# Optimization experiments

Hardware: AMD Instinct MI355X
Metric: run time of the kernel (lower is better)

## Reference

```python
import jax, jax.numpy as jnp
import numpy as np

WS = 7           # window_size
DIM_HEAD = 32    # qk head dim
NUM_HEAD = 8     # dim_in // dim_head = 256 // 32
DIM_EXP = 1024   # dim_in * exp_ratio
WIN_NUM = 16     # (28 // 7) ** 2
EPS = 1e-5


def _rel_pos_index():
    # same construction as torch buffer; returns [49*49] int index into (2*WS-1)^2 table
    coords = np.stack(np.meshgrid(np.arange(WS), np.arange(WS), indexing='ij'))  # [2,WS,WS]
    cf = coords.reshape(2, -1)                                                   # [2,49]
    rel = cf[:, :, None] - cf[:, None, :]                                        # [2,49,49]
    rel = rel.transpose(1, 2, 0)
    rel[:, :, 0] += WS - 1
    rel[:, :, 1] += WS - 1
    rel[:, :, 0] *= 2 * WS - 1
    return jnp.asarray(rel.sum(-1).reshape(-1), dtype=jnp.int32)                 # [2401]


def _ln_channel(x, w, b):
    # LayerNorm over channel dim (axis=1) of [b,c,h,w], per the 'ln_1d' norm
    mu = jnp.mean(x, axis=1, keepdims=True)
    var = jnp.var(x, axis=1, keepdims=True)
    xn = (x - mu) * jax.lax.rsqrt(var + EPS)
    return xn * w[None, :, None, None] + b[None, :, None, None]


def setup_inputs() -> dict:
    key = jax.random.key(0)
    ks = jax.random.split(key, 12)
    C = 256
    x = jax.random.normal(ks[0], (64, C, 28, 28), dtype=jnp.float32)
    return {
        'x': x,
        'pre_w': jnp.ones((C,), jnp.float32),
        'pre_b': jnp.zeros((C,), jnp.float32),
        'qk_w': jax.random.normal(ks[1], (2 * C, C), jnp.float32) * 0.02,
        'qk_b': jnp.zeros((2 * C,), jnp.float32),
        'v_w': jax.random.normal(ks[2], (DIM_EXP, C), jnp.float32) * 0.02,
        'v_b': jnp.zeros((DIM_EXP,), jnp.float32),
        'post_w': jnp.ones((DIM_EXP // 2,), jnp.float32),
        'post_b': jnp.zeros((DIM_EXP // 2,), jnp.float32),
        'proj_w': jax.random.normal(ks[3], (C, DIM_EXP), jnp.float32) * 0.02,
        'proj_b': jnp.zeros((C,), jnp.float32),
        'rpb_table': jax.random.normal(ks[4], (WIN_NUM, (2 * WS - 1) ** 2, NUM_HEAD), jnp.float32) * 0.02,
    }


def reference(x, pre_w, pre_b, qk_w, qk_b, v_w, v_b, post_w, post_b, proj_w, proj_b, rpb_table):
    B, C, H, W = x.shape
    n1, n2 = H // WS, W // WS
    shortcut = x
    # b c (h1 n1) (w1 n2) -> (b n1 n2) c h1 w1
    xw = x.reshape(B, C, WS, n1, WS, n2).transpose(0, 3, 5, 1, 2, 4).reshape(B * n1 * n2, C, WS, WS)
    b = B * n1 * n2
    xw = _ln_channel(xw, pre_w, pre_b)
    # 1x1 conv QK -> split into q,k per head: channels ordered (qk, heads, dim_head)
    qk = jnp.einsum('oc,bchw->bohw', qk_w, xw) + qk_b[None, :, None, None]
    qk = qk.reshape(b, 2, NUM_HEAD, DIM_HEAD, WS * WS).transpose(1, 0, 2, 4, 3)  # [2,b,h,49,dh]
    q, k = qk[0], qk[1]
    # 1x1 conv V -> attn half + idle half
    v = jnp.einsum('oc,bchw->bohw', v_w, xw) + v_b[None, :, None, None]
    v_attn, v_idle = jnp.split(v, 2, axis=1)                                     # each [b,512,7,7]
    dhv = (DIM_EXP // 2) // NUM_HEAD
    va = v_attn.reshape(b, NUM_HEAD, dhv, WS * WS).transpose(0, 1, 3, 2)         # [b,h,49,dhv]
    # relative position bias (gathered fresh each forward, one table per window)
    idx = _rel_pos_index()
    bias = rpb_table[:, idx, :]                                                  # [wn,2401,nh]
    bias = bias.reshape(WIN_NUM, WS * WS, WS * WS, NUM_HEAD).transpose(0, 3, 1, 2)
    bias = jnp.broadcast_to(bias[None], (B, WIN_NUM, NUM_HEAD, WS * WS, WS * WS)).reshape(b, NUM_HEAD, WS * WS, WS * WS)
    # SDPA (scale = 1/sqrt(q head dim), additive float mask)
    scale = DIM_HEAD ** -0.5
    logits = jnp.einsum('bhqd,bhkd->bhqk', q, k) * scale + bias
    attn = jax.nn.softmax(logits, axis=-1)
    out = jnp.einsum('bhqk,bhkd->bhqd', attn, va)                                # [b,h,49,dhv]
    out = out.transpose(0, 1, 3, 2).reshape(b, DIM_EXP // 2, WS, WS)
    out = _ln_channel(out, post_w, post_b)
    xc = jnp.concatenate([out, v_idle], axis=1)                                  # [b,dim_exp,7,7]
    # (b n1 n2) c h1 w1 -> b c (h1 n1) (w1 n2)
    xc = xc.reshape(B, n1, n2, DIM_EXP, WS, WS).transpose(0, 3, 4, 1, 5, 2).reshape(B, DIM_EXP, H, W)
    xc = jax.nn.gelu(xc, approximate=False)
    xc = jnp.einsum('oc,bchw->bohw', proj_w, xc) + proj_b[None, :, None, None]
    y = shortcut + xc
    return jnp.roll(y, shift=(2, 2), axis=(2, 3))
```

## Files before the change

kernel.cpp:

```cpp
#include <hip/hip_runtime.h>
#include <hip/hip_bf16.h>

typedef __bf16          bf16x8 __attribute__((ext_vector_type(8)));
typedef float           f32x4  __attribute__((ext_vector_type(4)));
typedef unsigned int    u32x2  __attribute__((ext_vector_type(2)));
typedef unsigned int    u32x4v __attribute__((ext_vector_type(4)));

#define QKW_OFF  0
#define VW_OFF   262144
#define PJW_OFF  786432
#define BIAS_OFF 1310720
#define XT_OFF   70516736

#define MFMA(a,b,c) __builtin_amdgcn_mfma_f32_16x16x32_bf16((a),(b),(c),0,0,0)
#define ZERO4 ((f32x4){0.f,0.f,0.f,0.f})
#define CBAR() asm volatile("" ::: "memory")

#define SXN_AT(row, byte)      ((((row)*512 + (byte))) ^ ((((row)&7))<<4))
#define RGB(j)                 (25088 + (j)*6400)
#define RG_AT(base, row, byte) (((base) + (row)*128 + (byte)) ^ (((row)&7)<<4))
#define SC_AT(row, byte)       ((25088 + (row)*512 + (byte)) ^ (((row)&7)<<4))

static __device__ __forceinline__ unsigned cvtpk(float lo, float hi){
  unsigned r;
  asm("v_cvt_pk_bf16_f32 %0, %1, %2" : "=v"(r) : "v"(lo), "v"(hi));
  return r;
}
static __device__ __forceinline__ unsigned short f2bu(float f) {
  unsigned u = __builtin_bit_cast(unsigned, f);
  return (unsigned short)((u + 0x7FFFu + ((u >> 16) & 1u)) >> 16);
}
static __device__ __forceinline__ float gelu_f(float v){
  return v / (1.f + __expf(-1.5957691216057308f*v*(1.f + 0.044715f*v*v)));
}

__global__ void emo_prep_wb(const float* __restrict__ qk_w, const float* __restrict__ v_w,
                            const float* __restrict__ proj_w, const float* __restrict__ rpb,
                            unsigned short* __restrict__ w16, float* __restrict__ bx) {
  const int blk = blockIdx.x;
  if (blk < 2560) {
    int i = blk * 256 + threadIdx.x;
    if (i >= 655360) return;
    float v;
    if (i < 131072)      v = qk_w[i];
    else if (i < 393216) v = v_w[i - 131072];
    else                 v = proj_w[i - 393216];
    unsigned u = __builtin_bit_cast(unsigned, v);
    w16[i] = (unsigned short)((u + 0x7FFFu + ((u >> 16) & 1u)) >> 16);
  } else {
    const int wh = blk - 2560;
    const int win = wh >> 3, h = wh & 7;
    for (int e = threadIdx.x; e < 4096; e += 256) {
      const int chunk = e >> 8, lane = (e >> 2) & 63, r = e & 3;
      const int mt = chunk >> 2, nt = chunk & 3;
      const int m = mt*16 + (lane >> 4)*4 + r;
      const int n = nt*16 + (lane & 15);
      float v;
      if (n >= 49)      v = -1e30f;
      else if (m >= 49) v = 0.f;
      else {
        const int dI = m/7 - n/7 + 6;
        const int dJ = m%7 - n%7 + 6;
        v = rpb[(win*169 + dI*13 + dJ)*8 + h];
      }
      bx[wh*4096 + e] = v;
    }
  }
}

__global__ __launch_bounds__(256)
void emo_prep_x(const float* __restrict__ x, const float* __restrict__ pre_w,
                const float* __restrict__ pre_b, unsigned short* __restrict__ xt) {
  __shared__ float lv[32*257];
  __shared__ float ps1[8][32];
  __shared__ float ps2[8][32];
  const int tid = threadIdx.x, lane = tid & 63, wv = tid >> 6;
  const int l32 = lane & 31, hp = lane >> 5;
  const int chunk = blockIdx.x, b = blockIdx.y;
  const int s = chunk*32 + l32;
  const bool ok = s < 784;
  const float* xb = x + (size_t)b*200704;
  float s1 = 0.f, s2 = 0.f;
  const int c0 = wv*64 + hp*32;
  for (int ci = 0; ci < 32; ++ci) {
    const int c = c0 + ci;
    const float v = ok ? xb[c*784 + s] : 0.f;
    lv[l32*257 + c] = v;
    s1 += v; s2 += v*v;
  }
  ps1[wv*2 + hp][l32] = s1;
  ps2[wv*2 + hp][l32] = s2;
  __syncthreads();
  const int px = tid & 31, j = tid >> 5;
  const int sp = chunk*32 + px;
  if (sp < 784) {
    float t1 = 0.f, t2 = 0.f;
    #pragma unroll
    for (int k = 0; k < 8; ++k) { t1 += ps1[k][px]; t2 += ps2[k][px]; }
    const float mu = t1*(1.f/256.f);
    const float rs = rsqrtf(t2*(1.f/256.f) - mu*mu + 1e-5f);
    const int h = sp/28, w = sp - h*28;
    const int win = (h & 3)*4 + (w & 3);
    const int wpx = (h >> 2)*7 + (w >> 2);
    unsigned short* row = xt + (((size_t)b*16 + win)*49 + wpx)*256 + j*32;
    #pragma unroll
    for (int g = 0; g < 4; ++g) {
      float gg[8];
      #pragma unroll
      for (int i2 = 0; i2 < 8; ++i2) {
        const int c = j*32 + g*8 + i2;
        gg[i2] = (lv[px*257 + c] - mu)*rs*pre_w[c] + pre_b[c];
      }
      u32x4v pk = { cvtpk(gg[0],gg[1]), cvtpk(gg[2],gg[3]), cvtpk(gg[4],gg[5]), cvtpk(gg[6],gg[7]) };
      *(u32x4v*)(row + g*8) = pk;
    }
  }
}

__global__ __launch_bounds__(512, 4)
void emo_main(const float* __restrict__ x,
              const float* __restrict__ qk_b,  const float* __restrict__ v_b,
              const float* __restrict__ post_w,const float* __restrict__ post_b,
              const float* __restrict__ proj_b,
              const char*  __restrict__ wsc,
              float* __restrict__ out)
{
  extern __shared__ char smem[];
  const int tid  = threadIdx.x;
  const int lane = tid & 63;
  const int l16  = lane & 15;
  const int lk   = lane >> 4;
  const int wv   = tid >> 6;
  const int bid  = blockIdx.x;
  const int Bi   = (bid & 7) * 8 + (bid >> 7);
  const int win  = (bid >> 3) & 15;
  const int n1   = win >> 2, n2 = win & 3;
  const size_t xbase = (size_t)Bi * (256*784);
  const int SCR  = RGB(wv);

  {
    const unsigned short* xw = (const unsigned short*)(wsc + XT_OFF)
                             + ((size_t)Bi*16 + win)*(49*256);
    for (int p = wv; p < 49; p += 8) {
      const u32x2 d = *(const u32x2*)(xw + p*256 + lane*4);
      *(u32x2*)(smem + SXN_AT(p, lane*8)) = d;
    }
  }
  __syncthreads();

  f32x4 aq[2][4], ak[2][4];
  #pragma unroll
  for (int mt = 0; mt < 2; ++mt)
    #pragma unroll
    for (int nt = 0; nt < 4; ++nt) { aq[mt][nt] = ZERO4; ak[mt][nt] = ZERO4; }
  #pragma unroll 2
  for (int kt = 0; kt < 8; ++kt) {
    bf16x8 bx[4];
    #pragma unroll
    for (int nt = 0; nt < 4; ++nt) {
      const int row = nt*16 + l16, rc = row < 49 ? row : 48;
      bx[nt] = *(const bf16x8*)(smem + SXN_AT(rc, kt*64 + lk*16));
    }
    #pragma unroll
    for (int mt = 0; mt < 2; ++mt) {
      const bf16x8 awq = *(const bf16x8*)(wsc + QKW_OFF + (size_t)(      wv*32 + mt*16 + l16)*512 + kt*64 + lk*16);
      const bf16x8 awk = *(const bf16x8*)(wsc + QKW_OFF + (size_t)(256 + wv*32 + mt*16 + l16)*512 + kt*64 + lk*16);
      #pragma unroll
      for (int nt = 0; nt < 4; ++nt) {
        aq[mt][nt] = MFMA(awq, bx[nt], aq[mt][nt]);
        ak[mt][nt] = MFMA(awk, bx[nt], ak[mt][nt]);
      }
    }
  }
  {
    const f32x4 bq0 = *(const f32x4*)(qk_b +       wv*32 +      lk*4);
    const f32x4 bq1 = *(const f32x4*)(qk_b +       wv*32 + 16 + lk*4);
    const f32x4 bk0 = *(const f32x4*)(qk_b + 256 + wv*32 +      lk*4);
    const f32x4 bk1 = *(const f32x4*)(qk_b + 256 + wv*32 + 16 + lk*4);
    #pragma unroll
    for (int nt = 0; nt < 4; ++nt) {
      aq[0][nt] += bq0; aq[1][nt] += bq1; ak[0][nt] += bk0; ak[1][nt] += bk1;
    }
  }

  #pragma unroll
  for (int nt = 0; nt < 4; ++nt) {
    const int px = nt*16 + l16;
    if (px < 49) {
      #pragma unroll
      for (int mt = 0; mt < 2; ++mt) {
        u32x2 pq  = { cvtpk(aq[mt][nt][0], aq[mt][nt][1]), cvtpk(aq[mt][nt][2], aq[mt][nt][3]) };
        u32x2 pk2 = { cvtpk(ak[mt][nt][0], ak[mt][nt][1]), cvtpk(ak[mt][nt][2], ak[mt][nt][3]) };
        *(u32x2*)(smem + RG_AT(SCR, px,      (mt*16 + lk*4)*2)) = pq;
        *(u32x2*)(smem + RG_AT(SCR, px, 64 + (mt*16 + lk*4)*2)) = pk2;
      }
    }
  }
  CBAR();

  bf16x8 qa[4], kb[4];
  #pragma unroll
  for (int t = 0; t < 4; ++t) {
    const int row = t*16 + l16, rc = row < 49 ? row : 48;
    qa[t] = *(const bf16x8*)(smem + RG_AT(SCR, rc,      lk*16));
    kb[t] = *(const bf16x8*)(smem + RG_AT(SCR, rc, 64 + lk*16));
  }

  f32x4 s[4][4];
  {
    const float scale = 0.17677669529663689f;
    const float* bxp = (const float*)(wsc + BIAS_OFF) + (size_t)(win*8 + wv)*4096 + lane*4;
    #pragma unroll
    for (int mt = 0; mt < 4; ++mt)
      #pragma unroll
      for (int nt = 0; nt < 4; ++nt) {
        f32x4 z = MFMA(qa[mt], kb[nt], ZERO4);
        s[mt][nt] = z*scale + *(const f32x4*)(bxp + (mt*4 + nt)*256);
      }
  }
  #pragma unroll
  for (int mt = 0; mt < 4; ++mt) {
    #pragma unroll
    for (int r = 0; r < 4; ++r) {
      float mx = fmaxf(fmaxf(s[mt][0][r], s[mt][1][r]), fmaxf(s[mt][2][r], s[mt][3][r]));
      mx = fmaxf(mx, __shfl_xor(mx, 1)); mx = fmaxf(mx, __shfl_xor(mx, 2));
      mx = fmaxf(mx, __shfl_xor(mx, 4)); mx = fmaxf(mx, __shfl_xor(mx, 8));
      const float e0 = __expf(s[mt][0][r]-mx), e1 = __expf(s[mt][1][r]-mx);
      const float e2 = __expf(s[mt][2][r]-mx), e3 = __expf(s[mt][3][r]-mx);
      float sm = e0+e1+e2+e3;
      sm += __shfl_xor(sm, 1); sm += __shfl_xor(sm, 2);
      sm += __shfl_xor(sm, 4); sm += __shfl_xor(sm, 8);
      const float inv = 1.f/sm;
      s[mt][0][r] = e0*inv; s[mt][1][r] = e1*inv;
      s[mt][2][r] = e2*inv; s[mt][3][r] = e3*inv;
    }
  }
  #pragma unroll
  for (int mt = 0; mt < 4; ++mt)
    #pragma unroll
    for (int r = 0; r < 4; ++r) {
      const int q = mt*16 + lk*4 + r;
      if (q < 49) {
        #pragma unroll
        for (int nt = 0; nt < 4; ++nt)
          *(unsigned short*)(smem + RG_AT(SCR, q, (nt*16 + l16)*2)) = f2bu(s[mt][nt][r]);
      }
    }
  CBAR();

  f32x4 av[4][4];
  #pragma unroll
  for (int mt = 0; mt < 4; ++mt)
    #pragma unroll
    for (int nt = 0; nt < 4; ++nt) av[mt][nt] = ZERO4;
  #pragma unroll 2
  for (int kt = 0; kt < 8; ++kt) {
    bf16x8 ax[4], bw[4];
    #pragma unroll
    for (int t = 0; t < 4; ++t) {
      const int row = t*16 + l16, rc = row < 49 ? row : 48;
      ax[t] = *(const bf16x8*)(smem + SXN_AT(rc, kt*64 + lk*16));
      bw[t] = *(const bf16x8*)(wsc + VW_OFF + (size_t)(wv*64 + t*16 + l16)*512 + kt*64 + lk*16);
    }
    #pragma unroll
    for (int mt = 0; mt < 4; ++mt)
      #pragma unroll
      for (int nt = 0; nt < 4; ++nt) av[mt][nt] = MFMA(ax[mt], bw[nt], av[mt][nt]);
  }
  {
    #pragma unroll
    for (int nt = 0; nt < 4; ++nt) {
      const float vb = v_b[wv*64 + nt*16 + l16];
      #pragma unroll
      for (int mt = 0; mt < 4; ++mt)
        #pragma unroll
        for (int r = 0; r < 4; ++r) av[mt][nt][r] += vb;
    }
  }

  bf16x8 fpb[4][2];
  #pragma unroll
  for (int t = 0; t < 4; ++t) {
    const int row = t*16 + l16, rc = row < 49 ? row : 48;
    #pragma unroll
    for (int kt = 0; kt < 2; ++kt)
      fpb[t][kt] = *(const bf16x8*)(smem + RG_AT(SCR, rc, (kt*32 + lk*8)*2));
  }
  CBAR();

  f32x4 o[4][4];
  #pragma unroll
  for (int h2 = 0; h2 < 2; ++h2) {
    #pragma unroll
    for (int tc = 0; tc < 2; ++tc) {
      const int nt = h2*2 + tc;
      const int chrow = tc*16 + l16;
      #pragma unroll
      for (int mt = 0; mt < 4; ++mt) {
        u32x2 pv = { cvtpk(av[mt][nt][0], av[mt][nt][1]), cvtpk(av[mt][nt][2], av[mt][nt][3]) };
        *(u32x2*)(smem + RG_AT(SCR, chrow, (mt*16 + lk*4)*2)) = pv;
      }
    }
    CBAR();
    #pragma unroll
    for (int tc = 0; tc < 2; ++tc) {
      const int mtc = h2*2 + tc;
      const bf16x8 a0 = *(const bf16x8*)(smem + RG_AT(SCR, tc*16 + l16, (     lk*8)*2));
      const bf16x8 a1 = *(const bf16x8*)(smem + RG_AT(SCR, tc*16 + l16, (32 + lk*8)*2));
      #pragma unroll
      for (int nt = 0; nt < 4; ++nt) {
        f32x4 z = MFMA(a0, fpb[nt][0], ZERO4);
        o[mtc][nt] = MFMA(a1, fpb[nt][1], z);
      }
    }
    CBAR();
  }

  #pragma unroll
  for (int mtc = 0; mtc < 4; ++mtc)
    #pragma unroll
    for (int nt = 0; nt < 4; ++nt) {
      const int q = nt*16 + l16;
      if (q < 49) {
        u32x2 pk = { cvtpk(o[mtc][nt][0], o[mtc][nt][1]), cvtpk(o[mtc][nt][2], o[mtc][nt][3]) };
        *(u32x2*)(smem + RG_AT(RGB(wv), q, (mtc*16 + lk*4)*2)) = pk;
      }
    }
  __syncthreads();

  {
    const int px = tid >> 3, j = tid & 7;
    if (px < 49) {
      bf16x8 f[8];
      float s1 = 0.f, s2 = 0.f;
      #pragma unroll
      for (int c8 = 0; c8 < 8; ++c8) {
        f[c8] = *(const bf16x8*)(smem + RG_AT(RGB(j), px, c8*16));
        #pragma unroll
        for (int i = 0; i < 8; ++i) { const float v = (float)f[c8][i]; s1 += v; s2 += v*v; }
      }
      s1 += __shfl_xor(s1, 1); s1 += __shfl_xor(s1, 2); s1 += __shfl_xor(s1, 4);
      s2 += __shfl_xor(s2, 1); s2 += __shfl_xor(s2, 2); s2 += __shfl_xor(s2, 4);
      const float mu = s1*(1.f/512.f);
      const float rs = rsqrtf(s2*(1.f/512.f) - mu*mu + 1e-5f);
      #pragma unroll
      for (int c8 = 0; c8 < 8; ++c8) {
        const f32x4 pw0 = *(const f32x4*)(post_w + j*64 + c8*8);
        const f32x4 pw1 = *(const f32x4*)(post_w + j*64 + c8*8 + 4);
        const f32x4 pb0 = *(const f32x4*)(post_b + j*64 + c8*8);
        const f32x4 pb1 = *(const f32x4*)(post_b + j*64 + c8*8 + 4);
        float g[8];
        #pragma unroll
        for (int i = 0; i < 8; ++i) {
          const float v = (float)f[c8][i];
          const float w = i < 4 ? pw0[i] : pw1[i-4];
          const float b = i < 4 ? pb0[i] : pb1[i-4];
          g[i] = gelu_f((v-mu)*rs*w + b);
        }
        u32x4v pk = { cvtpk(g[0],g[1]), cvtpk(g[2],g[3]), cvtpk(g[4],g[5]), cvtpk(g[6],g[7]) };
        *(u32x4v*)(smem + RG_AT(RGB(j), px, c8*16)) = pk;
      }
    }
  }
  __syncthreads();

  f32x4 pacc[2][4];
  #pragma unroll
  for (int mt = 0; mt < 2; ++mt)
    #pragma unroll
    for (int nt = 0; nt < 4; ++nt) pacc[mt][nt] = ZERO4;
  for (int j8 = 0; j8 < 8; ++j8) {
    #pragma unroll
    for (int kt2 = 0; kt2 < 2; ++kt2) {
      bf16x8 b[4];
      #pragma unroll
      for (int nt = 0; nt < 4; ++nt) {
        const int row = nt*16 + l16, rc = row < 49 ? row : 48;
        b[nt] = *(const bf16x8*)(smem + RG_AT(RGB(j8), rc, (kt2*32 + lk*8)*2));
      }
      const int kg = j8*64 + kt2*32 + lk*8;
      #pragma unroll
      for (int mt = 0; mt < 2; ++mt) {
        const bf16x8 aw = *(const bf16x8*)(wsc + PJW_OFF + (size_t)(wv*32 + mt*16 + l16)*2048 + kg*2);
        #pragma unroll
        for (int nt = 0; nt < 4; ++nt) pacc[mt][nt] = MFMA(aw, b[nt], pacc[mt][nt]);
      }
    }
  }
  for (int half = 0; half < 2; ++half) {
    __syncthreads();
    f32x4 ia[2][4];
    #pragma unroll
    for (int mt = 0; mt < 2; ++mt)
      #pragma unroll
      for (int nt = 0; nt < 4; ++nt) ia[mt][nt] = ZERO4;
    const int r0 = 512 + half*256 + wv*32;
    #pragma unroll 2
    for (int kt = 0; kt < 8; ++kt) {
      bf16x8 b[4];
      #pragma unroll
      for (int nt = 0; nt < 4; ++nt) {
        const int row = nt*16 + l16, rc = row < 49 ? row : 48;
        b[nt] = *(const bf16x8*)(smem + SXN_AT(rc, kt*64 + lk*16));
      }
      #pragma unroll
      for (int mt = 0; mt < 2; ++mt) {
        const bf16x8 aw = *(const bf16x8*)(wsc + VW_OFF + (size_t)(r0 + mt*16 + l16)*512 + kt*64 + lk*16);
        #pragma unroll
        for (int nt = 0; nt < 4; ++nt) ia[mt][nt] = MFMA(aw, b[nt], ia[mt][nt]);
      }
    }
    #pragma unroll
    for (int mt = 0; mt < 2; ++mt) {
      const f32x4 vb = *(const f32x4*)(v_b + r0 + mt*16 + lk*4);
      #pragma unroll
      for (int nt = 0; nt < 4; ++nt) {
        const int px = nt*16 + l16;
        const int chl = wv*32 + mt*16 + lk*4;
        u32x2 pk = { cvtpk(gelu_f(ia[mt][nt][0]+vb[0]), gelu_f(ia[mt][nt][1]+vb[1])),
                     cvtpk(gelu_f(ia[mt][nt][2]+vb[2]), gelu_f(ia[mt][nt][3]+vb[3])) };
        *(u32x2*)(smem + SC_AT(px, chl*2)) = pk;
      }
    }
    __syncthreads();
    #pragma unroll 2
    for (int kt = 0; kt < 8; ++kt) {
      bf16x8 b[4];
      #pragma unroll
      for (int nt = 0; nt < 4; ++nt) {
        const int row = nt*16 + l16;
        b[nt] = *(const bf16x8*)(smem + SC_AT(row, (kt*32 + lk*8)*2));
      }
      const int kg = 512 + half*256 + kt*32 + lk*8;
      #pragma unroll
      for (int mt = 0; mt < 2; ++mt) {
        const bf16x8 aw = *(const bf16x8*)(wsc + PJW_OFF + (size_t)(wv*32 + mt*16 + l16)*2048 + kg*2);
        #pragma unroll
        for (int nt = 0; nt < 4; ++nt) pacc[mt][nt] = MFMA(aw, b[nt], pacc[mt][nt]);
      }
    }
  }

  {
    int xoff[4], roff[4];
    #pragma unroll
    for (int nt = 0; nt < 4; ++nt) {
      const int px = nt*16 + l16;
      const int pc = px < 49 ? px : 48;
      const int gh = (pc/7)*4 + n1, gw = (pc%7)*4 + n2;
      xoff[nt] = gh*28 + gw;
      int rh = gh + 2; if (rh >= 28) rh -= 28;
      int rw = gw + 2; if (rw >= 28) rw -= 28;
      roff[nt] = rh*28 + rw;
    }
    #pragma unroll
    for (int mt = 0; mt < 2; ++mt) {
      #pragma unroll
      for (int r = 0; r < 4; ++r) {
        const int o2 = wv*32 + mt*16 + lk*4 + r;
        const float pb = proj_b[o2];
        const size_t cb = xbase + (size_t)o2*784;
        #pragma unroll
        for (int nt = 0; nt < 4; ++nt) {
          if (nt*16 + l16 < 49)
            out[cb + roff[nt]] = x[cb + xoff[nt]] + pacc[mt][nt][r] + pb;
        }
      }
    }
  }
}

extern "C" void kernel_launch(void* const* d_in, const int* in_sizes, int n_in,
                              void* d_out, int out_size, void* d_ws, size_t ws_size,
                              hipStream_t stream) {
  const float* x      = (const float*)d_in[0];
  const float* pre_w  = (const float*)d_in[1];
  const float* pre_b  = (const float*)d_in[2];
  const float* qk_w   = (const float*)d_in[3];
  const float* qk_b   = (const float*)d_in[4];
  const float* v_w    = (const float*)d_in[5];
  const float* v_b    = (const float*)d_in[6];
  const float* post_w = (const float*)d_in[7];
  const float* post_b = (const float*)d_in[8];
  const float* proj_w = (const float*)d_in[9];
  const float* proj_b = (const float*)d_in[10];
  const float* rpb    = (const float*)d_in[11];
  float* outp = (float*)d_out;
  char* wsc = (char*)d_ws;

  hipFuncSetAttribute((const void*)emo_main, hipFuncAttributeMaxDynamicSharedMemorySize, 81920);

  emo_prep_wb<<<2688, 256, 0, stream>>>(qk_w, v_w, proj_w, rpb,
                                        (unsigned short*)wsc, (float*)(wsc + BIAS_OFF));
  emo_prep_x<<<dim3(25, 64), 256, 0, stream>>>(x, pre_w, pre_b,
                                               (unsigned short*)(wsc + XT_OFF));
  emo_main<<<1024, 512, 76288, stream>>>(x, qk_b, v_b, post_w, post_b, proj_b,
                                         (const char*)wsc, outp);
}
```

Before: 290.1 us.

## Merge prep kernels, prefetch first QK weights, single-pass idle-V GELU into proj

The two preprocessing kernels become one launch, with block ranges dispatching to x-normalization, weight conversion or bias expansion, which removes a kernel launch and its gap. In the main kernel the first k-slice of QK weights is loaded before the x staging barrier so the global load overlaps with the LDS fill. The idle-V half is now computed in a single pass of 64 rows per wave, not two halves of 32 rows. Its GELU output goes into the per-wave regions reused from attention, and the projection reads them like the attention output, which drops one barrier pair and the separate scratch layout. This raises register pressure (16 accumulators per wave for V) and adds a px<49 guard on the stores.

```diff
diff --git a/kernel.cpp b/kernel.cpp
--- a/kernel.cpp
+++ b/kernel.cpp
@@ -19,7 +19,6 @@
 #define SXN_AT(row, byte)      ((((row)*512 + (byte))) ^ ((((row)&7))<<4))
 #define RGB(j)                 (25088 + (j)*6400)
 #define RG_AT(base, row, byte) (((base) + (row)*128 + (byte)) ^ (((row)&7)<<4))
-#define SC_AT(row, byte)       ((25088 + (row)*512 + (byte)) ^ (((row)&7)<<4))
 
 static __device__ __forceinline__ unsigned cvtpk(float lo, float hi){
   unsigned r;
@@ -34,49 +33,52 @@
   return v / (1.f + __expf(-1.5957691216057308f*v*(1.f + 0.044715f*v*v)));
 }
 
-__global__ void emo_prep_wb(const float* __restrict__ qk_w, const float* __restrict__ v_w,
-                            const float* __restrict__ proj_w, const float* __restrict__ rpb,
-                            unsigned short* __restrict__ w16, float* __restrict__ bx) {
+__global__ __launch_bounds__(256)
+void emo_prep(const float* __restrict__ x, const float* __restrict__ pre_w,
+              const float* __restrict__ pre_b,
+              const float* __restrict__ qk_w, const float* __restrict__ v_w,
+              const float* __restrict__ proj_w, const float* __restrict__ rpb,
+              unsigned short* __restrict__ xt,
+              unsigned short* __restrict__ w16, float* __restrict__ bx) {
   const int blk = blockIdx.x;
-  if (blk < 2560) {
-    int i = blk * 256 + threadIdx.x;
-    if (i >= 655360) return;
-    float v;
-    if (i < 131072)      v = qk_w[i];
-    else if (i < 393216) v = v_w[i - 131072];
-    else                 v = proj_w[i - 393216];
-    unsigned u = __builtin_bit_cast(unsigned, v);
-    w16[i] = (unsigned short)((u + 0x7FFFu + ((u >> 16) & 1u)) >> 16);
-  } else {
-    const int wh = blk - 2560;
-    const int win = wh >> 3, h = wh & 7;
-    for (int e = threadIdx.x; e < 4096; e += 256) {
-      const int chunk = e >> 8, lane = (e >> 2) & 63, r = e & 3;
-      const int mt = chunk >> 2, nt = chunk & 3;
-      const int m = mt*16 + (lane >> 4)*4 + r;
-      const int n = nt*16 + (lane & 15);
+  const int tid = threadIdx.x;
+  if (blk >= 1600) {
+    if (blk < 4160) {
+      int i = (blk - 1600) * 256 + tid;
+      if (i >= 655360) return;
       float v;
-      if (n >= 49)      v = -1e30f;
-      else if (m >= 49) v = 0.f;
-      else {
-        const int dI = m/7 - n/7 + 6;
-        const int dJ = m%7 - n%7 + 6;
-        v = rpb[(win*169 + dI*13 + dJ)*8 + h];
-      }
-      bx[wh*4096 + e] = v;
-    }
-  }
-}
-
-__global__ __launch_bounds__(256)
-void emo_prep_x(const float* __restrict__ x, const float* __restrict__ pre_w,
-                const float* __restrict__ pre_b, unsigned short* __restrict__ xt) {
+      if (i < 131072)      v = qk_w[i];
+      else if (i < 393216) v = v_w[i - 131072];
+      else                 v = proj_w[i - 393216];
+      unsigned u = __builtin_bit_cast(unsigned, v);
+      w16[i] = (unsigned short)((u + 0x7FFFu + ((u >> 16) & 1u)) >> 16);
+    } else {
+      const int wh = blk - 4160;
+      const int win = wh >> 3, h = wh & 7;
+      for (int e = tid; e < 4096; e += 256) {
+        const int chunk = e >> 8, lane = (e >> 2) & 63, r = e & 3;
+        const int mt = chunk >> 2, nt = chunk & 3;
+        const int m = mt*16 + (lane >> 4)*4 + r;
+        const int n = nt*16 + (lane & 15);
+        float v;
+        if (n >= 49)      v = -1e30f;
+        else if (m >= 49) v = 0.f;
+        else {
+          const int dI = m/7 - n/7 + 6;
+          const int dJ = m%7 - n%7 + 6;
+          v = rpb[(win*169 + dI*13 + dJ)*8 + h];
+        }
+        bx[wh*4096 + e] = v;
+      }
+    }
+    return;
+  }
   __shared__ float lv[32*257];
   __shared__ float ps1[8][32];
   __shared__ float ps2[8][32];
-  const int tid = threadIdx.x, lane = tid & 63, wv = tid >> 6;
+  const int lane = tid & 63, wv = tid >> 6;
   const int l32 = lane & 31, hp = lane >> 5;
-  const int chunk = blockIdx.x, b = blockIdx.y;
+  const int chunk = blk % 25, b = blk / 25;
   const int s = chunk*32 + l32;
   const bool ok = s < 784;
   const float* xb = x + (size_t)b*200704;
@@ -138,6 +140,13 @@
   const size_t xbase = (size_t)Bi * (256*784);
   const int SCR  = RGB(wv);
 
+  bf16x8 awq0[2], awk0[2];
+  #pragma unroll
+  for (int mt = 0; mt < 2; ++mt) {
+    awq0[mt] = *(const bf16x8*)(wsc + QKW_OFF + (size_t)(      wv*32 + mt*16 + l16)*512 + lk*16);
+    awk0[mt] = *(const bf16x8*)(wsc + QKW_OFF + (size_t)(256 + wv*32 + mt*16 + l16)*512 + lk*16);
+  }
+
   {
     const unsigned short* xw = (const unsigned short*)(wsc + XT_OFF)
                              + ((size_t)Bi*16 + win)*(49*256);
@@ -149,12 +158,23 @@
   __syncthreads();
 
   f32x4 aq[2][4], ak[2][4];
-  #pragma unroll
-  for (int mt = 0; mt < 2; ++mt)
-    #pragma unroll
-    for (int nt = 0; nt < 4; ++nt) { aq[mt][nt] = ZERO4; ak[mt][nt] = ZERO4; }
+  {
+    bf16x8 bx[4];
+    #pragma unroll
+    for (int nt = 0; nt < 4; ++nt) {
+      const int row = nt*16 + l16, rc = row < 49 ? row : 48;
+      bx[nt] = *(const bf16x8*)(smem + SXN_AT(rc, lk*16));
+    }
+    #pragma unroll
+    for (int mt = 0; mt < 2; ++mt)
+      #pragma unroll
+      for (int nt = 0; nt < 4; ++nt) {
+        aq[mt][nt] = MFMA(awq0[mt], bx[nt], ZERO4);
+        ak[mt][nt] = MFMA(awk0[mt], bx[nt], ZERO4);
+      }
+  }
   #pragma unroll 2
-  for (int kt = 0; kt < 8; ++kt) {
+  for (int kt = 1; kt < 8; ++kt) {
     bf16x8 bx[4];
     #pragma unroll
     for (int nt = 0; nt < 4; ++nt) {
@@ -387,51 +407,54 @@
       }
     }
   }
-  for (int half = 0; half < 2; ++half) {
-    __syncthreads();
-    f32x4 ia[2][4];
-    #pragma unroll
-    for (int mt = 0; mt < 2; ++mt)
+
+  __syncthreads();
+  {
+    f32x4 ia[4][4];
+    #pragma unroll
+    for (int mt = 0; mt < 4; ++mt)
       #pragma unroll
       for (int nt = 0; nt < 4; ++nt) ia[mt][nt] = ZERO4;
-    const int r0 = 512 + half*256 + wv*32;
     #pragma unroll 2
     for (int kt = 0; kt < 8; ++kt) {
+      bf16x8 b[4], aw[4];
+      #pragma unroll
+      for (int t = 0; t < 4; ++t) {
+        const int row = t*16 + l16, rc = row < 49 ? row : 48;
+        b[t]  = *(const bf16x8*)(smem + SXN_AT(rc, kt*64 + lk*16));
+        aw[t] = *(const bf16x8*)(wsc + VW_OFF + (size_t)(512 + wv*64 + t*16 + l16)*512 + kt*64 + lk*16);
+      }
+      #pragma unroll
+      for (int mt = 0; mt < 4; ++mt)
+        #pragma unroll
+        for (int nt = 0; nt < 4; ++nt) ia[mt][nt] = MFMA(aw[mt], b[nt], ia[mt][nt]);
+    }
+    #pragma unroll
+    for (int mt = 0; mt < 4; ++mt) {
+      const f32x4 vb = *(const f32x4*)(v_b + 512 + wv*64 + mt*16 + lk*4);
+      #pragma unroll
+      for (int nt = 0; nt < 4; ++nt) {
+        const int px = nt*16 + l16;
+        if (px < 49) {
+          u32x2 pk = { cvtpk(gelu_f(ia[mt][nt][0]+vb[0]), gelu_f(ia[mt][nt][1]+vb[1])),
+                       cvtpk(gelu_f(ia[mt][nt][2]+vb[2]), gelu_f(ia[mt][nt][3]+vb[3])) };
+          *(u32x2*)(smem + RG_AT(RGB(wv), px, (mt*16 + lk*4)*2)) = pk;
+        }
+      }
+    }
+  }
+  __syncthreads();
+
+  for (int j8 = 0; j8 < 8; ++j8) {
+    #pragma unroll
+    for (int kt2 = 0; kt2 < 2; ++kt2) {
       bf16x8 b[4];
       #pragma unroll
       for (int nt = 0; nt < 4; ++nt) {
         const int row = nt*16 + l16, rc = row < 49 ? row : 48;
-        b[nt] = *(const bf16x8*)(smem + SXN_AT(rc, kt*64 + lk*16));
-      }
-      #pragma unroll
-      for (int mt = 0; mt < 2; ++mt) {
-        const bf16x8 aw = *(const bf16x8*)(wsc + VW_OFF + (size_t)(r0 + mt*16 + l16)*512 + kt*64 + lk*16);
-        #pragma unroll
-        for (int nt = 0; nt < 4; ++nt) ia[mt][nt] = MFMA(aw, b[nt], ia[mt][nt]);
-      }
-    }
-    #pragma unroll
-    for (int mt = 0; mt < 2; ++mt) {
-      const f32x4 vb = *(const f32x4*)(v_b + r0 + mt*16 + lk*4);
-      #pragma unroll
-      for (int nt = 0; nt < 4; ++nt) {
-        const int px = nt*16 + l16;
-        const int chl = wv*32 + mt*16 + lk*4;
-        u32x2 pk = { cvtpk(gelu_f(ia[mt][nt][0]+vb[0]), gelu_f(ia[mt][nt][1]+vb[1])),
-                     cvtpk(gelu_f(ia[mt][nt][2]+vb[2]), gelu_f(ia[mt][nt][3]+vb[3])) };
-        *(u32x2*)(smem + SC_AT(px, chl*2)) = pk;
-      }
-    }
-    __syncthreads();
-    #pragma unroll 2
-    for (int kt = 0; kt < 8; ++kt) {
-      bf16x8 b[4];
-      #pragma unroll
-      for (int nt = 0; nt < 4; ++nt) {
-        const int row = nt*16 + l16;
-        b[nt] = *(const bf16x8*)(smem + SC_AT(row, (kt*32 + lk*8)*2));
-      }
-      const int kg = 512 + half*256 + kt*32 + lk*8;
+        b[nt] = *(const bf16x8*)(smem + RG_AT(RGB(j8), rc, (kt2*32 + lk*8)*2));
+      }
+      const int kg = 512 + j8*64 + kt2*32 + lk*8;
       #pragma unroll
       for (int mt = 0; mt < 2; ++mt) {
         const bf16x8 aw = *(const bf16x8*)(wsc + PJW_OFF + (size_t)(wv*32 + mt*16 + l16)*2048 + kg*2);
@@ -490,10 +513,9 @@
 
   hipFuncSetAttribute((const void*)emo_main, hipFuncAttributeMaxDynamicSharedMemorySize, 81920);
 
-  emo_prep_wb<<<2688, 256, 0, stream>>>(qk_w, v_w, proj_w, rpb,
-                                        (unsigned short*)wsc, (float*)(wsc + BIAS_OFF));
-  emo_prep_x<<<dim3(25, 64), 256, 0, stream>>>(x, pre_w, pre_b,
-                                               (unsigned short*)(wsc + XT_OFF));
+  emo_prep<<<4288, 256, 0, stream>>>(x, pre_w, pre_b, qk_w, v_w, proj_w, rpb,
+                                     (unsigned short*)(wsc + XT_OFF),
+                                     (unsigned short*)wsc, (float*)(wsc + BIAS_OFF));
   emo_main<<<1024, 512, 76288, stream>>>(x, qk_b, v_b, post_w, post_b, proj_b,
                                          (const char*)wsc, outp);
 }
```

Result: slower. 352.8 us (+21.6%).
